# Kernel tuning notes

Hardware: AMD Instinct MI355X
Metric: run time of the kernel (lower is better)

The kernel has to match this reference:

```python
import jax, jax.numpy as jnp
import numpy as np

V, F_IN, H, DH, T = 512, 8, 64, 4, 3
E, P, L = 8192, 64, 8
D = H + DH  # path-decoder GRU width


def setup_inputs() -> dict:
    key = jax.random.key(0)
    ks = jax.random.split(key, 24)
    s = 0.1
    inp = {
        "adj_matrix": jax.random.normal(ks[0], (V, V, F_IN), jnp.float32),
        "edges": jax.random.randint(ks[1], (E, 2), 0, V),
        "paths": jax.random.randint(ks[2], (P, L), 0, V),
        "demands": jax.random.uniform(ks[3], (P,), jnp.float32),
        "emb_w": jax.random.normal(ks[4], (H, F_IN), jnp.float32) * s,
        "w1s": jax.random.normal(ks[5], (T, H, H), jnp.float32) * s,
        "w2s": jax.random.normal(ks[6], (T, H, H), jnp.float32) * s,
        "w3s": jax.random.normal(ks[7], (T, H, H), jnp.float32) * s,
        "gru_w_ih": jax.random.normal(ks[8], (3 * H, 2 * H), jnp.float32) * s,
        "gru_w_hh": jax.random.normal(ks[9], (3 * H, H), jnp.float32) * s,
        "gru_b_ih": jax.random.normal(ks[10], (3 * H,), jnp.float32) * s,
        "gru_b_hh": jax.random.normal(ks[11], (3 * H,), jnp.float32) * s,
        "pf_w_ih": jax.random.normal(ks[12], (3 * D, D), jnp.float32) * s,
        "pf_w_hh": jax.random.normal(ks[13], (3 * D, D), jnp.float32) * s,
        "pf_b_ih": jax.random.normal(ks[14], (3 * D,), jnp.float32) * s,
        "pf_b_hh": jax.random.normal(ks[15], (3 * D,), jnp.float32) * s,
        "pb_w_ih": jax.random.normal(ks[16], (3 * D, D), jnp.float32) * s,
        "pb_w_hh": jax.random.normal(ks[17], (3 * D, D), jnp.float32) * s,
        "pb_b_ih": jax.random.normal(ks[18], (3 * D,), jnp.float32) * s,
        "pb_b_hh": jax.random.normal(ks[19], (3 * D,), jnp.float32) * s,
        "wq": jax.random.normal(ks[20], (1, D), jnp.float32) * s,
        "bq": jax.random.normal(ks[21], (1,), jnp.float32) * s,
        "wd": jax.random.normal(ks[22], (DH, 1), jnp.float32) * s,
    }
    return inp


def _gru(x_seq, h0, w_ih, w_hh, b_ih, b_hh):
    """torch-style GRU, batch_first. x_seq (B,Tn,I), h0 (B,Hd) -> (ys, h_last)."""
    def step(h, x_t):
        gi = x_t @ w_ih.T + b_ih
        gh = h @ w_hh.T + b_hh
        ir, iz, inn = jnp.split(gi, 3, axis=-1)
        hr, hz, hn = jnp.split(gh, 3, axis=-1)
        r = jax.nn.sigmoid(ir + hr)
        z = jax.nn.sigmoid(iz + hz)
        n = jnp.tanh(inn + r * hn)
        h_new = (1.0 - z) * n + z * h
        return h_new, h_new
    h_last, ys = jax.lax.scan(step, h0, jnp.swapaxes(x_seq, 0, 1))
    return jnp.swapaxes(ys, 0, 1), h_last


def _message_passing(x, u, v, w1, w2, w3):
    """Vectorized form of the per-edge python loop. x (V,V,Hd), u/v (E,)."""
    Hd = x.shape[-1]
    col_sum = x.sum(axis=0)                      # (V,Hd): sum over first index
    nz_row = jnp.sum(x != 0, axis=-1)            # (V,V) nonzero count per entry
    col_nz = nz_row.sum(axis=0)                  # (V,)
    # incoming edges for edge (u,v): column u, row v zeroed, mean over nonzeros
    s_in = col_sum[u] - x[v, u]                  # (E,Hd)
    n_in = (col_nz[u] - nz_row[v, u]).astype(x.dtype) / Hd
    n_in = jnp.where(n_in == 0, 1.0, n_in)
    e_in = s_in / n_in[:, None]
    # outgoing edges: reversed edge (v,u) -> column v, row u zeroed
    s_out = col_sum[v] - x[u, v]
    n_out = (col_nz[v] - nz_row[u, v]).astype(x.dtype) / Hd
    n_out = jnp.where(n_out == 0, 1.0, n_out)
    e_out = s_out / n_out[:, None]
    m = jax.nn.relu(x[u, v] @ w1.T + e_in @ w2.T + e_out @ w3.T)
    return x.at[u, v].set(m)


def reference(adj_matrix, edges, paths, demands, emb_w, w1s, w2s, w3s,
              gru_w_ih, gru_w_hh, gru_b_ih, gru_b_hh,
              pf_w_ih, pf_w_hh, pf_b_ih, pf_b_hh,
              pb_w_ih, pb_w_hh, pb_b_ih, pb_b_hh, wq, bq, wd):
    u, v = edges[:, 0], edges[:, 1]
    x = adj_matrix @ emb_w.T                     # (V,V,H)
    for t in range(T):
        m = _message_passing(x, u, v, w1s[t], w2s[t], w3s[t])
        inp = jnp.concatenate([m, x], axis=-1)   # (V,V,2H)
        x, _ = _gru(inp, jnp.zeros((x.shape[0], H), x.dtype),
                    gru_w_ih, gru_w_hh, gru_b_ih, gru_b_hh)
    demand_emb = jax.nn.relu(demands[:, None] @ wd.T)        # (P,DH)
    graph_emb = jnp.concatenate([x.mean(axis=(0, 1)),
                                 jnp.zeros((DH,), x.dtype)])  # (D,)
    src, dst = paths[:, :-1], paths[:, 1:]                    # (P,L-1)
    edge_feat = x[src, dst]                                   # (P,L-1,H)
    dem = jnp.broadcast_to(demand_emb[:, None, :], (P, L - 1, DH))
    feat = jnp.concatenate([edge_feat, dem], axis=-1)         # (P,L-1,D)
    h0 = jnp.broadcast_to(graph_emb, (P, D))
    _, hf = _gru(feat, h0, pf_w_ih, pf_w_hh, pf_b_ih, pf_b_hh)
    _, hb = _gru(feat[:, ::-1], h0, pb_w_ih, pb_w_hh, pb_b_ih, pb_b_hh)
    paths_emb = (hf + hb) * 0.5                               # mean over directions
    return jax.nn.softmax(paths_emb @ wq.T + bq, axis=0)      # (P,1)
```

## Files before the change

kernel.cpp:

```cpp
#include <hip/hip_runtime.h>


__device__ __forceinline__ float fsig_(float x) { return 1.f / (1.f + __expf(-x)); }
__device__ __forceinline__ float ftanh_(float x) {
  float e = __expf(2.f * x);
  return 1.f - 2.f / (e + 1.f);
}
__device__ __forceinline__ float sig_(float x) { return 1.f / (1.f + expf(-x)); }

__device__ __forceinline__ void barrier_lgkm() {
  asm volatile("s_waitcnt lgkmcnt(0)\n\ts_barrier" ::: "memory");
}

#define PIN4(v) asm volatile("" : "+v"((v).x), "+v"((v).y), "+v"((v).z), "+v"((v).w))

#define LD4(p) (*(const float4*)(p))
#define DOT4(acc, va, vb)                                                      \
  do {                                                                         \
    acc += (va).x * (vb).x; acc += (va).y * (vb).y;                            \
    acc += (va).z * (vb).z; acc += (va).w * (vb).w;                            \
  } while (0)

#define ALL16(M) M(0) M(1) M(2) M(3) M(4) M(5) M(6) M(7)                       \
                 M(8) M(9) M(10) M(11) M(12) M(13) M(14) M(15)
#define ALLQ(M) M(0,0) M(1,1) M(2,2) M(3,3) M(4,0) M(5,1) M(6,2) M(7,3)        \
                M(8,0) M(9,1) M(10,2) M(11,3) M(12,0) M(13,1) M(14,2) M(15,3)

__global__ __launch_bounds__(256) void embed_kernel(
    const float* __restrict__ adj, const float* __restrict__ emb,
    float* __restrict__ x)
{
  const int64_t row = (int64_t)blockIdx.x * 4 + (threadIdx.x >> 6);
  const int h = threadIdx.x & 63;
  const float* a = adj + row * 8;
  float acc = 0.f;
#pragma unroll
  for (int f = 0; f < 8; ++f) acc += a[f] * emb[h * 8 + f];
  x[row * 64 + h] = acc;
}

__global__ __launch_bounds__(256) void colsum_kernel(
    const float* __restrict__ x, float* __restrict__ col_sum,
    int* __restrict__ col_nz)
{
  const int j = blockIdx.x;
  const int h = threadIdx.x & 63;
  const int w = threadIdx.x >> 6;
  float acc = 0.f;
  int nz = 0;
  for (int i = w; i < 512; i += 4) {
    float v = x[((int64_t)i * 512 + j) * 64 + h];
    acc += v;
    nz += (v != 0.f) ? 1 : 0;
  }
  __shared__ float pacc[4][64];
  __shared__ int pnz[4];
#pragma unroll
  for (int off = 32; off > 0; off >>= 1) nz += __shfl_down(nz, off, 64);
  if (h == 0) pnz[w] = nz;
  pacc[w][h] = acc;
  __syncthreads();
  if (w == 0) {
    col_sum[j * 64 + h] = pacc[0][h] + pacc[1][h] + pacc[2][h] + pacc[3][h];
    if (h == 0) col_nz[j] = pnz[0] + pnz[1] + pnz[2] + pnz[3];
  }
}

__global__ void scatter_idx_kernel(const int* __restrict__ edges,
                                   int* __restrict__ idxmap)
{
  const int e = blockIdx.x * 256 + threadIdx.x;
  if (e < 8192) idxmap[edges[e * 2] * 512 + edges[e * 2 + 1]] = e;
}

__global__ __launch_bounds__(256) void edge_kernel(
    const float* __restrict__ x, const int* __restrict__ edges,
    const float* __restrict__ col_sum, const int* __restrict__ col_nz,
    const float* __restrict__ w1, const float* __restrict__ w2,
    const float* __restrict__ w3, const float* __restrict__ w_ih,
    float* __restrict__ delta_gi)
{
  const int wv = threadIdx.x >> 6;
  const int e = blockIdx.x * 4 + wv;
  const int h = threadIdx.x & 63;
  const int u = edges[e * 2 + 0];
  const int v = edges[e * 2 + 1];
  __shared__ __align__(16) float xuv[4][64], ein[4][64], eout[4][64], dm[4][64];
  const float xuvh = x[((int64_t)u * 512 + v) * 64 + h];
  const float xvuh = x[((int64_t)v * 512 + u) * 64 + h];
  xuv[wv][h] = xuvh;
  const int nz_vu = __popcll(__ballot(xvuh != 0.f));
  const int nz_uv = __popcll(__ballot(xuvh != 0.f));
  float n_in = (float)(col_nz[u] - nz_vu) / 64.f;
  if (n_in == 0.f) n_in = 1.f;
  float n_out = (float)(col_nz[v] - nz_uv) / 64.f;
  if (n_out == 0.f) n_out = 1.f;
  ein[wv][h] = (col_sum[u * 64 + h] - xvuh) / n_in;
  eout[wv][h] = (col_sum[v * 64 + h] - xuvh) / n_out;
  __syncthreads();
  const float4* w1r = (const float4*)(w1 + h * 64);
  const float4* w2r = (const float4*)(w2 + h * 64);
  const float4* w3r = (const float4*)(w3 + h * 64);
  const float4* xuv4 = (const float4*)&xuv[wv][0];
  const float4* ein4 = (const float4*)&ein[wv][0];
  const float4* eout4 = (const float4*)&eout[wv][0];
  float acc = 0.f;
#pragma unroll
  for (int kk = 0; kk < 16; ++kk) {
    float4 a = xuv4[kk], b = w1r[kk];
    acc += a.x * b.x + a.y * b.y + a.z * b.z + a.w * b.w;
    a = ein4[kk]; b = w2r[kk];
    acc += a.x * b.x + a.y * b.y + a.z * b.z + a.w * b.w;
    a = eout4[kk]; b = w3r[kk];
    acc += a.x * b.x + a.y * b.y + a.z * b.z + a.w * b.w;
  }
  const float m = fmaxf(acc, 0.f);
  dm[wv][h] = m - xuvh;
  __syncthreads();
  const float4* dm4 = (const float4*)&dm[wv][0];
#pragma unroll
  for (int r = 0; r < 3; ++r) {
    const int gg = h + r * 64;
    const float4* wr = (const float4*)(w_ih + gg * 128);
    float d = 0.f;
#pragma unroll
    for (int kk = 0; kk < 16; ++kk) {
      float4 a = dm4[kk], b = wr[kk];
      d += a.x * b.x + a.y * b.y + a.z * b.z + a.w * b.w;
    }
    delta_gi[e * 192 + gg] = d;
  }
}

#define DECL_W(i)                                                              \
  float4 W##i; {                                                               \
    float4 t0 = LD4(wg + 4 * (i));                                             \
    float4 t1 = LD4(wg + 64 + 4 * (i));                                        \
    W##i.x = t0.x + t1.x; W##i.y = t0.y + t1.y;                                \
    W##i.z = t0.z + t1.z; W##i.w = t0.w + t1.w;                                \
  }                                                                            \
  PIN4(W##i);
#define DECL_X(i) float4 X##i = LD4(xrow + 4 * (i));
#define PQ(i, q) { DOT4(ac##q, X##i, W##i); X##i = LD4(xnext + 4 * (i)); }
#define DECL_WR(i) float4 WR##i = LD4(wr_ + 4 * (i)); PIN4(WR##i);
#define DECL_WZ(i) float4 WZ##i = LD4(wz_ + 4 * (i)); PIN4(WZ##i);
#define DECL_WN(i) float4 WN##i = LD4(wn_ + 4 * (i)); PIN4(WN##i);
#define CCHUNK(i)                                                              \
  { float4 hc = hs4[(i)];                                                      \
    DOT4(racc, hc, WR##i); DOT4(zacc, hc, WZ##i); DOT4(nacc, hc, WN##i); }

__global__ __launch_bounds__(256, 2) void scan_kernel(
    float* __restrict__ x, const float* __restrict__ delta_gi,
    const int* __restrict__ idxmap,
    const float* __restrict__ w_ih, const float* __restrict__ w_hh,
    const float* __restrict__ b_ih, const float* __restrict__ b_hh)
{
  const int b = blockIdx.x;
  const int tid = threadIdx.x;
  __shared__ __align__(16) float hs[64];
  __shared__ float gib[2][192];
  __shared__ int idxl[512];
  float* xrow = x + (int64_t)b * 32768;

  for (int i = tid; i < 512; i += 256) idxl[i] = idxmap[b * 512 + i];

  if (tid < 192) {
    const int g = tid;
    const float* wg = w_ih + g * 128;
    ALL16(DECL_W)
    const float bi = b_ih[g];
    ALL16(DECL_X)
    __syncthreads();
    {
      float ac0 = bi, ac1 = 0.f, ac2 = 0.f, ac3 = 0.f;
      const float* xnext = xrow + 64;
      ALLQ(PQ)
      float acc = (ac0 + ac1) + (ac2 + ac3);
      const int i0 = idxl[0];
      if (i0 >= 0) acc += delta_gi[(int64_t)i0 * 192 + g];
      gib[0][g] = acc;
    }
    const int idx1 = idxl[1];
    float dgn = 0.f;
    if (idx1 >= 0) dgn = delta_gi[(int64_t)idx1 * 192 + g];
    barrier_lgkm();
    for (int t = 0; t < 512; ++t) {
      if (t < 511) {
        const int tn2 = (t + 2 < 512) ? (t + 2) : 511;
        const float* xnext = xrow + tn2 * 64;
        float ac0 = bi + dgn, ac1 = 0.f, ac2 = 0.f, ac3 = 0.f;
        ALLQ(PQ)
        gib[(t + 1) & 1][g] = (ac0 + ac1) + (ac2 + ac3);
        const int idxn = idxl[tn2];
        dgn = 0.f;
        if (idxn >= 0) dgn = delta_gi[(int64_t)idxn * 192 + g];
      }
      barrier_lgkm();
    }
  } else {
    const int j = tid - 192;
    const float* wr_ = w_hh + j * 64;
    const float* wz_ = w_hh + (j + 64) * 64;
    const float* wn_ = w_hh + (j + 128) * 64;
    ALL16(DECL_WR)
    ALL16(DECL_WZ)
    ALL16(DECL_WN)
    const float bhr = b_hh[j], bhz = b_hh[j + 64], bhn = b_hh[j + 128];
    float hj = 0.f;
    hs[j] = 0.f;
    __syncthreads();
    __builtin_amdgcn_s_setprio(1);
    barrier_lgkm();
    const float4* hs4 = (const float4*)hs;
    for (int t = 0; t < 512; ++t) {
      const float gr = gib[t & 1][j];
      const float gz = gib[t & 1][64 + j];
      const float gn = gib[t & 1][128 + j];
      float racc = bhr, zacc = bhz, nacc = bhn;
      ALL16(CCHUNK)
      const float r = fsig_(gr + racc);
      const float z = fsig_(gz + zacc);
      const float n = ftanh_(gn + r * nacc);
      hj = (1.f - z) * n + z * hj;
      hs[j] = hj;
      xrow[t * 64 + j] = hj;
      barrier_lgkm();
    }
  }
}

__global__ __launch_bounds__(256) void path_kernel(
    const float* __restrict__ x, const int* __restrict__ paths,
    const float* __restrict__ demands, const float* __restrict__ wd,
    const float* __restrict__ col_sum,
    const float* __restrict__ wih_f, const float* __restrict__ whh_f,
    const float* __restrict__ bih_f, const float* __restrict__ bhh_f,
    const float* __restrict__ wih_b, const float* __restrict__ whh_b,
    const float* __restrict__ bih_b, const float* __restrict__ bhh_b,
    float* __restrict__ h_out)
{
  const int p = blockIdx.x & 63;
  const int dir = blockIdx.x >> 6;
  const int g = threadIdx.x;
  const float* w_ih = dir ? wih_b : wih_f;
  const float* w_hh = dir ? whh_b : whh_f;
  const float* bih = dir ? bih_b : bih_f;
  const float* bhh = dir ? bhh_b : bhh_f;
  __shared__ float feat[7][68], hs[68], rbuf[68], zbuf[68];
  if (g < 64) {
    float s = 0.f;
#pragma unroll 8
    for (int jj = 0; jj < 512; ++jj) s += col_sum[jj * 64 + g];
    hs[g] = s * (1.f / 262144.f);
  } else if (g < 68) {
    hs[g] = 0.f;
  }
  if (g < 68) {
#pragma unroll
    for (int t = 0; t < 7; ++t) {
      const int src = paths[p * 8 + t];
      const int dst = paths[p * 8 + t + 1];
      feat[t][g] = (g < 64) ? x[((int64_t)src * 512 + dst) * 64 + g]
                            : fmaxf(demands[p] * wd[g - 64], 0.f);
    }
  }
  __syncthreads();
  for (int s = 0; s < 7; ++s) {
    const int t = dir ? (6 - s) : s;
    float acc = 0.f, hacc = 0.f;
    if (g < 204) {
      acc = bih[g];
      hacc = bhh[g];
      for (int k = 0; k < 68; ++k) {
        acc += feat[t][k] * w_ih[g * 68 + k];
        hacc += hs[k] * w_hh[g * 68 + k];
      }
    }
    if (g < 68) rbuf[g] = sig_(acc + hacc);
    else if (g < 136) zbuf[g - 68] = sig_(acc + hacc);
    __syncthreads();
    if (g >= 136 && g < 204) {
      const int j = g - 136;
      const float n = tanhf(acc + rbuf[j] * hacc);
      const float z = zbuf[j];
      const float hn = (1.f - z) * n + z * hs[j];
      hs[j] = hn;
    }
    __syncthreads();
  }
  if (g < 68) h_out[(dir * 64 + p) * 68 + g] = hs[g];
}

__global__ __launch_bounds__(64) void combine_kernel(
    const float* __restrict__ h_out, const float* __restrict__ wq,
    const float* __restrict__ bq, float* __restrict__ out)
{
  const int p = threadIdx.x;
  float l = bq[0];
#pragma unroll
  for (int d = 0; d < 68; ++d)
    l += 0.5f * (h_out[p * 68 + d] + h_out[(64 + p) * 68 + d]) * wq[d];
  float mx = l;
#pragma unroll
  for (int off = 32; off > 0; off >>= 1) mx = fmaxf(mx, __shfl_xor(mx, off, 64));
  const float e = expf(l - mx);
  float s = e;
#pragma unroll
  for (int off = 32; off > 0; off >>= 1) s += __shfl_xor(s, off, 64);
  out[p] = e / s;
}

extern "C" void kernel_launch(void* const* d_in, const int* in_sizes, int n_in,
                              void* d_out, int out_size, void* d_ws, size_t ws_size,
                              hipStream_t stream)
{
  const float* adj = (const float*)d_in[0];
  const int* edges = (const int*)d_in[1];
  const int* paths = (const int*)d_in[2];
  const float* demands = (const float*)d_in[3];
  const float* emb_w = (const float*)d_in[4];
  const float* w1s = (const float*)d_in[5];
  const float* w2s = (const float*)d_in[6];
  const float* w3s = (const float*)d_in[7];
  const float* gru_w_ih = (const float*)d_in[8];
  const float* gru_w_hh = (const float*)d_in[9];
  const float* gru_b_ih = (const float*)d_in[10];
  const float* gru_b_hh = (const float*)d_in[11];
  const float* pf_w_ih = (const float*)d_in[12];
  const float* pf_w_hh = (const float*)d_in[13];
  const float* pf_b_ih = (const float*)d_in[14];
  const float* pf_b_hh = (const float*)d_in[15];
  const float* pb_w_ih = (const float*)d_in[16];
  const float* pb_w_hh = (const float*)d_in[17];
  const float* pb_b_ih = (const float*)d_in[18];
  const float* pb_b_hh = (const float*)d_in[19];
  const float* wq = (const float*)d_in[20];
  const float* bq = (const float*)d_in[21];
  const float* wd = (const float*)d_in[22];
  float* out = (float*)d_out;

  float* xA = (float*)d_ws;
  float* col_sum = xA + 16777216;
  int* col_nz = (int*)(col_sum + 32768);
  int* idxmap = col_nz + 512;
  float* delta_gi = (float*)(idxmap + 262144);
  float* h_out = delta_gi + 1572864;

  hipMemsetAsync(idxmap, 0xFF, 262144 * sizeof(int), stream);
  scatter_idx_kernel<<<32, 256, 0, stream>>>(edges, idxmap);
  embed_kernel<<<65536, 256, 0, stream>>>(adj, emb_w, xA);

  for (int t = 0; t < 3; ++t) {
    colsum_kernel<<<512, 256, 0, stream>>>(xA, col_sum, col_nz);
    edge_kernel<<<2048, 256, 0, stream>>>(xA, edges, col_sum, col_nz,
        w1s + t * 4096, w2s + t * 4096, w3s + t * 4096, gru_w_ih, delta_gi);
    scan_kernel<<<512, 256, 0, stream>>>(xA, delta_gi, idxmap,
        gru_w_ih, gru_w_hh, gru_b_ih, gru_b_hh);
  }

  colsum_kernel<<<512, 256, 0, stream>>>(xA, col_sum, col_nz);
  path_kernel<<<128, 256, 0, stream>>>(xA, paths, demands, wd, col_sum,
      pf_w_ih, pf_w_hh, pf_b_ih, pf_b_hh,
      pb_w_ih, pb_w_hh, pb_b_ih, pb_b_hh, h_out);
  combine_kernel<<<1, 64, 0, stream>>>(h_out, wq, bq, out);
}
```

Measured before the change: 1.862 ms.

## Batch 16 GRU rows per block and compute gates with bf16 MFMA

Replaces the per-row scalar GRU scan (512 blocks, one row each, producer/consumer warp split) with a kernel in which each block handles 16 rows. Input and hidden projections are computed together with bf16 16x16x32 MFMA instructions, using weights held in registers. This removes the scalar FP32 dot-product cost of the sequential recurrence. In exchange it uses only 32 blocks, which leaves most CUs idle, and it rounds activations, hidden state and weights to bf16, which can cause precision drift across 512 recurrent steps.

```diff
diff --git a/kernel.cpp b/kernel.cpp
--- a/kernel.cpp
+++ b/kernel.cpp
@@ -1,5 +1,8 @@
 #include <hip/hip_runtime.h>
 
+
+typedef __attribute__((ext_vector_type(8))) short bf16x8;
+typedef __attribute__((ext_vector_type(4))) float f32x4;
 
 __device__ __forceinline__ float fsig_(float x) { return 1.f / (1.f + __expf(-x)); }
 __device__ __forceinline__ float ftanh_(float x) {
@@ -8,23 +11,19 @@
 }
 __device__ __forceinline__ float sig_(float x) { return 1.f / (1.f + expf(-x)); }
 
+__device__ __forceinline__ unsigned short f2bf(float f) {
+  union { float f; unsigned u; } a; a.f = f;
+  unsigned r = a.u + 0x7FFFu + ((a.u >> 16) & 1u);
+  return (unsigned short)(r >> 16);
+}
+
 __device__ __forceinline__ void barrier_lgkm() {
   asm volatile("s_waitcnt lgkmcnt(0)\n\ts_barrier" ::: "memory");
 }
 
-#define PIN4(v) asm volatile("" : "+v"((v).x), "+v"((v).y), "+v"((v).z), "+v"((v).w))
+#define MFMA16(a, b, c) __builtin_amdgcn_mfma_f32_16x16x32_bf16((a), (b), (c), 0, 0, 0)
 
 #define LD4(p) (*(const float4*)(p))
-#define DOT4(acc, va, vb)                                                      \
-  do {                                                                         \
-    acc += (va).x * (vb).x; acc += (va).y * (vb).y;                            \
-    acc += (va).z * (vb).z; acc += (va).w * (vb).w;                            \
-  } while (0)
-
-#define ALL16(M) M(0) M(1) M(2) M(3) M(4) M(5) M(6) M(7)                       \
-                 M(8) M(9) M(10) M(11) M(12) M(13) M(14) M(15)
-#define ALLQ(M) M(0,0) M(1,1) M(2,2) M(3,3) M(4,0) M(5,1) M(6,2) M(7,3)        \
-                M(8,0) M(9,1) M(10,2) M(11,3) M(12,0) M(13,1) M(14,2) M(15,3)
 
 __global__ __launch_bounds__(256) void embed_kernel(
     const float* __restrict__ adj, const float* __restrict__ emb,
@@ -132,100 +131,115 @@
   }
 }
 
-#define DECL_W(i)                                                              \
-  float4 W##i; {                                                               \
-    float4 t0 = LD4(wg + 4 * (i));                                             \
-    float4 t1 = LD4(wg + 64 + 4 * (i));                                        \
-    W##i.x = t0.x + t1.x; W##i.y = t0.y + t1.y;                                \
-    W##i.z = t0.z + t1.z; W##i.w = t0.w + t1.w;                                \
-  }                                                                            \
-  PIN4(W##i);
-#define DECL_X(i) float4 X##i = LD4(xrow + 4 * (i));
-#define PQ(i, q) { DOT4(ac##q, X##i, W##i); X##i = LD4(xnext + 4 * (i)); }
-#define DECL_WR(i) float4 WR##i = LD4(wr_ + 4 * (i)); PIN4(WR##i);
-#define DECL_WZ(i) float4 WZ##i = LD4(wz_ + 4 * (i)); PIN4(WZ##i);
-#define DECL_WN(i) float4 WN##i = LD4(wn_ + 4 * (i)); PIN4(WN##i);
-#define CCHUNK(i)                                                              \
-  { float4 hc = hs4[(i)];                                                      \
-    DOT4(racc, hc, WR##i); DOT4(zacc, hc, WZ##i); DOT4(nacc, hc, WN##i); }
-
-__global__ __launch_bounds__(256, 2) void scan_kernel(
+__global__ __launch_bounds__(256) void scan_mfma_kernel(
     float* __restrict__ x, const float* __restrict__ delta_gi,
     const int* __restrict__ idxmap,
     const float* __restrict__ w_ih, const float* __restrict__ w_hh,
     const float* __restrict__ b_ih, const float* __restrict__ b_hh)
 {
-  const int b = blockIdx.x;
   const int tid = threadIdx.x;
-  __shared__ __align__(16) float hs[64];
-  __shared__ float gib[2][192];
-  __shared__ int idxl[512];
-  float* xrow = x + (int64_t)b * 32768;
-
-  for (int i = tid; i < 512; i += 256) idxl[i] = idxmap[b * 512 + i];
-
-  if (tid < 192) {
-    const int g = tid;
-    const float* wg = w_ih + g * 128;
-    ALL16(DECL_W)
-    const float bi = b_ih[g];
-    ALL16(DECL_X)
-    __syncthreads();
-    {
-      float ac0 = bi, ac1 = 0.f, ac2 = 0.f, ac3 = 0.f;
-      const float* xnext = xrow + 64;
-      ALLQ(PQ)
-      float acc = (ac0 + ac1) + (ac2 + ac3);
-      const int i0 = idxl[0];
-      if (i0 >= 0) acc += delta_gi[(int64_t)i0 * 192 + g];
-      gib[0][g] = acc;
-    }
-    const int idx1 = idxl[1];
-    float dgn = 0.f;
-    if (idx1 >= 0) dgn = delta_gi[(int64_t)idx1 * 192 + g];
+  const int wv = tid >> 6;
+  const int l = tid & 63;
+  const int cl = l & 15;
+  const int kg = l >> 4;
+  const int b0 = blockIdx.x * 16;
+  const int u = wv * 16 + cl;
+
+  __shared__ unsigned short h_lds[16 * 64];
+  __shared__ int idxl[16][512];
+
+  for (int i = tid; i < 8192; i += 256)
+    idxl[i >> 9][i & 511] = idxmap[(int64_t)(b0 + (i >> 9)) * 512 + (i & 511)];
+  for (int i = tid; i < 512; i += 256) ((unsigned*)h_lds)[i] = 0;
+
+  bf16x8 BXr0, BXr1, BXz0, BXz1, BXn0, BXn1;
+  bf16x8 BHr0, BHr1, BHz0, BHz1, BHn0, BHn1;
+  {
+    union { bf16x8 v; unsigned short s[8]; } t0, t1, t2, t3, t4, t5;
+#define FILLB(kst)                                                             \
+    _Pragma("unroll")                                                          \
+    for (int j = 0; j < 8; ++j) {                                              \
+      const int k = (kst) * 32 + kg * 8 + j;                                   \
+      t0.s[j] = f2bf(w_ih[u * 128 + k] + w_ih[u * 128 + 64 + k]);              \
+      t1.s[j] = f2bf(w_ih[(64 + u) * 128 + k] + w_ih[(64 + u) * 128 + 64 + k]);\
+      t2.s[j] = f2bf(w_ih[(128 + u) * 128 + k] +                               \
+                     w_ih[(128 + u) * 128 + 64 + k]);                          \
+      t3.s[j] = f2bf(w_hh[u * 64 + k]);                                        \
+      t4.s[j] = f2bf(w_hh[(64 + u) * 64 + k]);                                 \
+      t5.s[j] = f2bf(w_hh[(128 + u) * 64 + k]);                                \
+    }
+    FILLB(0)
+    BXr0 = t0.v; BXz0 = t1.v; BXn0 = t2.v;
+    BHr0 = t3.v; BHz0 = t4.v; BHn0 = t5.v;
+    FILLB(1)
+    BXr1 = t0.v; BXz1 = t1.v; BXn1 = t2.v;
+    BHr1 = t3.v; BHz1 = t4.v; BHn1 = t5.v;
+#undef FILLB
+  }
+  const float brz_r = b_ih[u] + b_hh[u];
+  const float brz_z = b_ih[64 + u] + b_hh[64 + u];
+  const float bin = b_ih[128 + u];
+  const float bhn = b_hh[128 + u];
+
+  const float* xarow = x + (int64_t)(b0 + cl) * 32768;
+  float4 XF0a = LD4(xarow + kg * 8);
+  float4 XF0b = LD4(xarow + kg * 8 + 4);
+  float4 XF1a = LD4(xarow + 32 + kg * 8);
+  float4 XF1b = LD4(xarow + 32 + kg * 8 + 4);
+  float ho[4] = {0.f, 0.f, 0.f, 0.f};
+  const int swz = (cl & 7) << 4;
+  __syncthreads();
+
+  for (int t = 0; t < 512; ++t) {
+    bf16x8 HA0 = *(const bf16x8*)((const char*)h_lds + cl * 128 +
+                                  ((kg * 16) ^ swz));
+    bf16x8 HA1 = *(const bf16x8*)((const char*)h_lds + cl * 128 +
+                                  ((64 + kg * 16) ^ swz));
+    float dR[4], dZ[4], dN[4];
+#pragma unroll
+    for (int i = 0; i < 4; ++i) {
+      const int idx = idxl[4 * kg + i][t];
+      if (idx >= 0) {
+        const float* dp = delta_gi + (int64_t)idx * 192;
+        dR[i] = dp[u]; dZ[i] = dp[64 + u]; dN[i] = dp[128 + u];
+      } else { dR[i] = 0.f; dZ[i] = 0.f; dN[i] = 0.f; }
+    }
+    union { bf16x8 v; unsigned short s[8]; } xa0, xa1;
+    xa0.s[0] = f2bf(XF0a.x); xa0.s[1] = f2bf(XF0a.y);
+    xa0.s[2] = f2bf(XF0a.z); xa0.s[3] = f2bf(XF0a.w);
+    xa0.s[4] = f2bf(XF0b.x); xa0.s[5] = f2bf(XF0b.y);
+    xa0.s[6] = f2bf(XF0b.z); xa0.s[7] = f2bf(XF0b.w);
+    xa1.s[0] = f2bf(XF1a.x); xa1.s[1] = f2bf(XF1a.y);
+    xa1.s[2] = f2bf(XF1a.z); xa1.s[3] = f2bf(XF1a.w);
+    xa1.s[4] = f2bf(XF1b.x); xa1.s[5] = f2bf(XF1b.y);
+    xa1.s[6] = f2bf(XF1b.z); xa1.s[7] = f2bf(XF1b.w);
+    f32x4 zz = {0.f, 0.f, 0.f, 0.f};
+    f32x4 aR = MFMA16(xa0.v, BXr0, zz); aR = MFMA16(xa1.v, BXr1, aR);
+    aR = MFMA16(HA0, BHr0, aR);         aR = MFMA16(HA1, BHr1, aR);
+    f32x4 aZ = MFMA16(xa0.v, BXz0, zz); aZ = MFMA16(xa1.v, BXz1, aZ);
+    aZ = MFMA16(HA0, BHz0, aZ);         aZ = MFMA16(HA1, BHz1, aZ);
+    f32x4 aNX = MFMA16(xa0.v, BXn0, zz); aNX = MFMA16(xa1.v, BXn1, aNX);
+    f32x4 aNH = MFMA16(HA0, BHn0, zz);   aNH = MFMA16(HA1, BHn1, aNH);
+    const int tn = (t + 1 < 512) ? t + 1 : 511;
+    XF0a = LD4(xarow + tn * 64 + kg * 8);
+    XF0b = LD4(xarow + tn * 64 + kg * 8 + 4);
+    XF1a = LD4(xarow + tn * 64 + 32 + kg * 8);
+    XF1b = LD4(xarow + tn * 64 + 32 + kg * 8 + 4);
     barrier_lgkm();
-    for (int t = 0; t < 512; ++t) {
-      if (t < 511) {
-        const int tn2 = (t + 2 < 512) ? (t + 2) : 511;
-        const float* xnext = xrow + tn2 * 64;
-        float ac0 = bi + dgn, ac1 = 0.f, ac2 = 0.f, ac3 = 0.f;
-        ALLQ(PQ)
-        gib[(t + 1) & 1][g] = (ac0 + ac1) + (ac2 + ac3);
-        const int idxn = idxl[tn2];
-        dgn = 0.f;
-        if (idxn >= 0) dgn = delta_gi[(int64_t)idxn * 192 + g];
-      }
-      barrier_lgkm();
-    }
-  } else {
-    const int j = tid - 192;
-    const float* wr_ = w_hh + j * 64;
-    const float* wz_ = w_hh + (j + 64) * 64;
-    const float* wn_ = w_hh + (j + 128) * 64;
-    ALL16(DECL_WR)
-    ALL16(DECL_WZ)
-    ALL16(DECL_WN)
-    const float bhr = b_hh[j], bhz = b_hh[j + 64], bhn = b_hh[j + 128];
-    float hj = 0.f;
-    hs[j] = 0.f;
-    __syncthreads();
-    __builtin_amdgcn_s_setprio(1);
+#pragma unroll
+    for (int i = 0; i < 4; ++i) {
+      const float r = fsig_(aR[i] + brz_r + dR[i]);
+      const float zg = fsig_(aZ[i] + brz_z + dZ[i]);
+      const float nn = ftanh_(aNX[i] + bin + dN[i] + r * (aNH[i] + bhn));
+      const float hn = (1.f - zg) * nn + zg * ho[i];
+      ho[i] = hn;
+      const int row = 4 * kg + i;
+      *(unsigned short*)((char*)h_lds + row * 128 +
+                         ((u * 2) ^ ((row & 7) << 4))) = f2bf(hn);
+      x[(int64_t)(b0 + row) * 32768 + t * 64 + u] = hn;
+    }
+    asm volatile("s_waitcnt vmcnt(4)" ::: "memory");
     barrier_lgkm();
-    const float4* hs4 = (const float4*)hs;
-    for (int t = 0; t < 512; ++t) {
-      const float gr = gib[t & 1][j];
-      const float gz = gib[t & 1][64 + j];
-      const float gn = gib[t & 1][128 + j];
-      float racc = bhr, zacc = bhz, nacc = bhn;
-      ALL16(CCHUNK)
-      const float r = fsig_(gr + racc);
-      const float z = fsig_(gz + zacc);
-      const float n = ftanh_(gn + r * nacc);
-      hj = (1.f - z) * n + z * hj;
-      hs[j] = hj;
-      xrow[t * 64 + j] = hj;
-      barrier_lgkm();
-    }
   }
 }
 
@@ -354,7 +368,7 @@
     colsum_kernel<<<512, 256, 0, stream>>>(xA, col_sum, col_nz);
     edge_kernel<<<2048, 256, 0, stream>>>(xA, edges, col_sum, col_nz,
         w1s + t * 4096, w2s + t * 4096, w3s + t * 4096, gru_w_ih, delta_gi);
-    scan_kernel<<<512, 256, 0, stream>>>(xA, delta_gi, idxmap,
+    scan_mfma_kernel<<<32, 256, 0, stream>>>(xA, delta_gi, idxmap,
         gru_w_ih, gru_w_hh, gru_b_ih, gru_b_hh);
   }
 
```

After: 2.435 ms. 30.8% more time.
